# Optimization experiments

Hardware: AMD Instinct MI355X
Metric: run time of the kernel (lower is better)

## Reference

```python
import jax, jax.numpy as jnp
import numpy as np

DIM = 1024
HEADS = 16
DIM_HEAD = 64
SCALE = DIM_HEAD ** -0.5


def setup_inputs() -> dict:
    key = jax.random.key(0)
    ks = jax.random.split(key, 7)
    init = lambda k, shape: jax.random.normal(k, shape, dtype=jnp.float32) * (shape[0] ** -0.5)
    return {
        "x": jax.random.normal(ks[0], (4, 4096, DIM), dtype=jnp.float32),
        "Wq": init(ks[1], (DIM, HEADS * DIM_HEAD)),
        "Wk": init(ks[2], (DIM, HEADS * DIM_HEAD)),
        "Wv": init(ks[3], (DIM, HEADS * DIM_HEAD)),
        "Wg": init(ks[4], (DIM, HEADS * DIM_HEAD)),
        "bg": jnp.zeros((HEADS * DIM_HEAD,), dtype=jnp.float32),
        "Wo": init(ks[5], (HEADS * DIM_HEAD, DIM)),
    }


def _split_heads(t):
    b, n, _ = t.shape
    return t.reshape(b, n, HEADS, DIM_HEAD).transpose(0, 2, 1, 3)  # b h n d


def reference(x, Wq, Wk, Wv, Wg, bg, Wo):
    # projections
    q = _split_heads(x @ Wq)
    k = _split_heads(x @ Wk)
    v = _split_heads(x @ Wv)
    g = _split_heads(x @ Wg + bg)

    # feature map + gate
    q = jax.nn.elu(q) + 1.0
    k = jax.nn.elu(k) + 1.0
    g = jax.nn.sigmoid(g)

    # linear attention: per-head kv state, no n x n scores
    kv = jnp.einsum("bhnd,bhne->bhde", k, v)          # [b,h,d,d]
    k_sum = k.sum(axis=-2)                              # [b,h,d]
    z = 1.0 / jnp.clip(jnp.einsum("bhnd,bhd->bhn", q, k_sum), 1e-6)
    out = jnp.einsum("bhnd,bhde->bhne", q * SCALE, kv)
    out = out * z[..., None] * g                        # [b,h,n,d]

    b, h, n, d = out.shape
    out = out.transpose(0, 2, 1, 3).reshape(b, n, h * d)
    return out @ Wo
```

## Files before the change

### kernel.cpp

```cpp
#include <hip/hip_runtime.h>
#include <math.h>

#define DIM 1024
#define SCALE 0.125f
#define NT 16

typedef __attribute__((ext_vector_type(8))) short bh8;
typedef __attribute__((ext_vector_type(4))) short bh4;
typedef __attribute__((ext_vector_type(4))) float f4v;

__device__ __forceinline__ unsigned short f2bf(float f) {
  unsigned u = __builtin_bit_cast(unsigned, f);
  return (unsigned short)((u + 0x7FFFu + ((u >> 16) & 1u)) >> 16);
}
__device__ __forceinline__ float bf2f(unsigned short u) {
  return __builtin_bit_cast(float, (unsigned)u << 16);
}
__device__ __forceinline__ float elu1(float v) {
  return v > 0.f ? v + 1.f : __expf(v);
}
__device__ __forceinline__ f4v mfma16(bh8 a, bh8 b, f4v c) {
  return __builtin_amdgcn_mfma_f32_16x16x32_bf16(a, b, c, 0, 0, 0);
}

typedef const void __attribute__((address_space(1)))* gas1_t;
typedef void __attribute__((address_space(3)))* las3_t;

__device__ __forceinline__ bh8 frag(const unsigned short* lds, int row, int k8) {
  const int q = ((row << 3) | k8) ^ (row & 7);
  return *reinterpret_cast<const bh8*>(lds + q * 8);
}

__device__ __forceinline__ void gll_tile(const unsigned short* g, int ldg,
                                         unsigned short* lds, int t) {
  const int lane = t & 63, w = t >> 6;
#pragma unroll
  for (int cc = 0; cc < 4; ++cc) {
    const int base = (w * 4 + cc) * 64;
    const int q = base + lane;
    const int c = q ^ ((q >> 3) & 7);
    __builtin_amdgcn_global_load_lds(
        (gas1_t)(const void*)(g + (size_t)(c >> 3) * ldg + (c & 7) * 8),
        (las3_t)(void*)(lds + (size_t)base * 8), 16, 0, 0);
  }
}

__global__ __launch_bounds__(256) void p0(const float* __restrict__ x,
                                          unsigned short* __restrict__ xb) {
  const size_t i = ((size_t)blockIdx.x * 256 + threadIdx.x) * 8;
  const float4 a = *reinterpret_cast<const float4*>(x + i);
  const float4 b = *reinterpret_cast<const float4*>(x + i + 4);
  bh8 v;
  v[0] = (short)f2bf(a.x); v[1] = (short)f2bf(a.y);
  v[2] = (short)f2bf(a.z); v[3] = (short)f2bf(a.w);
  v[4] = (short)f2bf(b.x); v[5] = (short)f2bf(b.y);
  v[6] = (short)f2bf(b.z); v[7] = (short)f2bf(b.w);
  *reinterpret_cast<bh8*>(xb + i) = v;
}

__global__ __launch_bounds__(256) void p1(
    const float* __restrict__ Wq, const float* __restrict__ Wk,
    const float* __restrict__ Wv, const float* __restrict__ Wg,
    const float* __restrict__ Wo, unsigned short* __restrict__ WallT,
    unsigned short* __restrict__ WoT) {
  const int m = blockIdx.z;
  const int tc = blockIdx.x, tr = blockIdx.y;
  const int t = threadIdx.x;
  const float* src = m == 0 ? Wq : m == 1 ? Wk : m == 2 ? Wv : m == 3 ? Wg : Wo;
  __shared__ float tile[64][65];
#pragma unroll
  for (int i = 0; i < 4; ++i) {
    const int idx = i * 256 + t;
    const int r = idx >> 4;
    const int c4 = (idx & 15) * 4;
    const float4 v = *reinterpret_cast<const float4*>(
        src + (size_t)(tr * 64 + r) * DIM + tc * 64 + c4);
    tile[r][c4] = v.x; tile[r][c4 + 1] = v.y;
    tile[r][c4 + 2] = v.z; tile[r][c4 + 3] = v.w;
  }
  __syncthreads();
  unsigned short* dst = (m < 4) ? WallT : WoT;
#pragma unroll
  for (int i = 0; i < 4; ++i) {
    const int idx = i * 256 + t;
    const int lc = idx >> 4;
    const int k4i = (idx & 15) * 4;
    const size_t drow = (m < 4) ? (size_t)(tc * 256 + m * 64 + lc)
                                : (size_t)(tc * 64 + lc);
    bh4 v;
#pragma unroll
    for (int jj = 0; jj < 4; ++jj) v[jj] = (short)f2bf(tile[k4i + jj][lc]);
    *reinterpret_cast<bh4*>(dst + drow * DIM + tr * 64 + k4i) = v;
  }
}

template <int MODE>
__global__ __launch_bounds__(512, 2) void gemm8(
    const unsigned short* __restrict__ gA,
    const unsigned short* __restrict__ gB, const float* __restrict__ bg,
    unsigned short* __restrict__ ob, float* __restrict__ of,
    float* __restrict__ kv_part, float* __restrict__ ksum_part) {
  const int t = threadIdx.x, lane = t & 63, w = t >> 6;
  const int wr = w >> 2, wc = w & 3, g4 = lane >> 4, c0 = lane & 15;
  const int nwg = gridDim.x;
  const int NBC = (MODE == 0) ? 16 : 4;
  const int rbn = nwg / NBC;
  const int bid = (int)blockIdx.x;
  const int xcd = bid & 7;
  const int idx = bid >> 3;
  const int bandsz = rbn >> 3;
  const int cb = idx / bandsz;
  const int rb = xcd * bandsz + (idx - cb * bandsz);

  constexpr int LDGA = (MODE == 0) ? 1024 : 4096;
  constexpr int ASTR = (MODE == 0) ? 64 : 256;
  constexpr int AOFF = (MODE == 0) ? 0 : 64;

  __shared__ __align__(16) unsigned short lds[65536];

  int offA[2], offB[2], dstc[2];
#pragma unroll
  for (int cc = 0; cc < 2; ++cc) {
    const int base = (w * 2 + cc) * 64;
    const int q = base + lane;
    const int c = q ^ ((q >> 3) & 7);
    offA[cc] = (c >> 3) * LDGA + (c & 7) * 8;
    offB[cc] = (c >> 3) * 1024 + (c & 7) * 8;
    dstc[cc] = base * 8;
  }
  const unsigned short* Abase = gA + (size_t)rb * 256 * LDGA + AOFF;
  const unsigned short* Bbase = gB + (size_t)cb * 256 * 1024;

#define SA(kt, half)                                                          \
  {                                                                           \
    _Pragma("unroll") for (int cc = 0; cc < 2; ++cc)                          \
        __builtin_amdgcn_global_load_lds(                                     \
            (gas1_t)(Abase + (size_t)(half) * 128 * LDGA + offA[cc] +         \
                     (kt) * ASTR),                                            \
            (las3_t)(lds + ((kt) & 1) * 16384 + (half) * 8192 + dstc[cc]),    \
            16, 0, 0);                                                        \
  }
#define SB(kt, half)                                                          \
  {                                                                           \
    _Pragma("unroll") for (int cc = 0; cc < 2; ++cc)                          \
        __builtin_amdgcn_global_load_lds(                                     \
            (gas1_t)(Bbase + (size_t)(half) * 128 * 1024 + offB[cc] +         \
                     (kt) * 64),                                              \
            (las3_t)(lds + 32768 + ((kt) & 1) * 16384 + (half) * 8192 +       \
                     dstc[cc]),                                               \
            16, 0, 0);                                                        \
  }

  f4v acc[8][4];
#pragma unroll
  for (int i = 0; i < 8; ++i)
#pragma unroll
    for (int j = 0; j < 4; ++j) acc[i][j] = (f4v){0.f, 0.f, 0.f, 0.f};

  SB(0, 0); SB(0, 1); SA(0, 0); SA(0, 1); SB(1, 0); SB(1, 1);

#pragma unroll 2
  for (int kt = 0; kt < NT; ++kt) {
    if (kt < NT - 1) {
      asm volatile("s_waitcnt vmcnt(4)" ::: "memory");
    } else {
      asm volatile("s_waitcnt vmcnt(0)" ::: "memory");
    }
    __builtin_amdgcn_sched_barrier(0);
    __builtin_amdgcn_s_barrier();
    const unsigned short* Ah = lds + (kt & 1) * 16384 + wr * 8192;
    const unsigned short* Bh =
        lds + 32768 + (kt & 1) * 16384 + (wc >> 1) * 8192;
    const int br0 = (wc & 1) * 64;

    bh8 bfr[4][2], a0[2][2];
#pragma unroll
    for (int nf = 0; nf < 4; ++nf)
#pragma unroll
      for (int kf = 0; kf < 2; ++kf)
        bfr[nf][kf] = frag(Bh, br0 + nf * 16 + c0, kf * 4 + g4);
#pragma unroll
    for (int i = 0; i < 2; ++i)
#pragma unroll
      for (int kf = 0; kf < 2; ++kf)
        a0[i][kf] = frag(Ah, i * 16 + c0, kf * 4 + g4);
    if (kt + 1 < NT) { SA(kt + 1, 0); SA(kt + 1, 1); }
    __builtin_amdgcn_s_barrier();
    __builtin_amdgcn_s_setprio(1);
#pragma unroll
    for (int i = 0; i < 2; ++i)
#pragma unroll
      for (int nf = 0; nf < 4; ++nf)
#pragma unroll
        for (int kf = 0; kf < 2; ++kf)
          acc[i][nf] = mfma16(bfr[nf][kf], a0[i][kf], acc[i][nf]);
    __builtin_amdgcn_s_setprio(0);
    __builtin_amdgcn_s_barrier();

    bh8 a1[2][2];
#pragma unroll
    for (int i = 0; i < 2; ++i)
#pragma unroll
      for (int kf = 0; kf < 2; ++kf)
        a1[i][kf] = frag(Ah, (2 + i) * 16 + c0, kf * 4 + g4);
    if (kt + 2 < NT) SB(kt + 2, 0);
    __builtin_amdgcn_s_barrier();
    __builtin_amdgcn_s_setprio(1);
#pragma unroll
    for (int i = 0; i < 2; ++i)
#pragma unroll
      for (int nf = 0; nf < 4; ++nf)
#pragma unroll
        for (int kf = 0; kf < 2; ++kf)
          acc[2 + i][nf] = mfma16(bfr[nf][kf], a1[i][kf], acc[2 + i][nf]);
    __builtin_amdgcn_s_setprio(0);
    __builtin_amdgcn_s_barrier();

    bh8 a2[2][2];
#pragma unroll
    for (int i = 0; i < 2; ++i)
#pragma unroll
      for (int kf = 0; kf < 2; ++kf)
        a2[i][kf] = frag(Ah, (4 + i) * 16 + c0, kf * 4 + g4);
    if (kt + 2 < NT) SB(kt + 2, 1);
    __builtin_amdgcn_s_barrier();
    __builtin_amdgcn_s_setprio(1);
#pragma unroll
    for (int i = 0; i < 2; ++i)
#pragma unroll
      for (int nf = 0; nf < 4; ++nf)
#pragma unroll
        for (int kf = 0; kf < 2; ++kf)
          acc[4 + i][nf] = mfma16(bfr[nf][kf], a2[i][kf], acc[4 + i][nf]);
    __builtin_amdgcn_s_setprio(0);
    __builtin_amdgcn_s_barrier();

    bh8 a3[2][2];
#pragma unroll
    for (int i = 0; i < 2; ++i)
#pragma unroll
      for (int kf = 0; kf < 2; ++kf)
        a3[i][kf] = frag(Ah, (6 + i) * 16 + c0, kf * 4 + g4);
    __builtin_amdgcn_s_barrier();
    __builtin_amdgcn_s_setprio(1);
#pragma unroll
    for (int i = 0; i < 2; ++i)
#pragma unroll
      for (int nf = 0; nf < 4; ++nf)
#pragma unroll
        for (int kf = 0; kf < 2; ++kf)
          acc[6 + i][nf] = mfma16(bfr[nf][kf], a3[i][kf], acc[6 + i][nf]);
    __builtin_amdgcn_s_setprio(0);
  }
#undef SA
#undef SB

  if (MODE == 0) {
    float bgv[4][4];
    if (wc == 3) {
#pragma unroll
      for (int nf = 0; nf < 4; ++nf) {
        const float4 bv =
            *reinterpret_cast<const float4*>(bg + cb * 64 + nf * 16 + g4 * 4);
        bgv[nf][0] = bv.x; bgv[nf][1] = bv.y;
        bgv[nf][2] = bv.z; bgv[nf][3] = bv.w;
      }
    }
    if (wc == 0 || wc == 3) {
#pragma unroll
      for (int rf = 0; rf < 8; ++rf) {
        const size_t row = (size_t)rb * 256 + wr * 128 + rf * 16 + c0;
#pragma unroll
        for (int nf = 0; nf < 4; ++nf) {
          ushort4 o;
#pragma unroll
          for (int r = 0; r < 4; ++r) {
            float v = acc[rf][nf][r];
            if (wc == 0) v = elu1(v);
            else v = 1.f / (1.f + __expf(-(v + bgv[nf][r])));
            ((unsigned short*)&o)[r] = f2bf(v);
          }
          *reinterpret_cast<ushort4*>(
              ob + row * 4096 + cb * 256 + wc * 64 + nf * 16 + g4 * 4) = o;
        }
      }
    }

    __syncthreads();
    if (wc == 1 || wc == 2) {
      unsigned short* dstT = lds + (wc == 2 ? 16896 : 0);
#pragma unroll
      for (int rf = 0; rf < 8; ++rf) {
        const int n = wr * 128 + rf * 16 + c0;
#pragma unroll
        for (int nf = 0; nf < 4; ++nf)
#pragma unroll
          for (int r = 0; r < 4; ++r) {
            float v = acc[rf][nf][r];
            if (wc == 1) v = elu1(v);
            dstT[(nf * 16 + g4 * 4 + r) * 264 + n] = f2bf(v);
          }
      }
    }
    __syncthreads();
    const unsigned short* kT = lds;
    const unsigned short* vT = lds + 16896;
    const size_t pbase = (size_t)((rb >> 4) * 16 + cb) * 16 + (rb & 15);
#pragma unroll
    for (int pi = 0; pi < 2; ++pi) {
      const int p = w * 2 + pi, dt = p >> 2, et = p & 3;
      f4v a = (f4v){0.f, 0.f, 0.f, 0.f};
#pragma unroll
      for (int kn = 0; kn < 8; ++kn) {
        const bh8 kq = *reinterpret_cast<const bh8*>(
            kT + (dt * 16 + c0) * 264 + kn * 32 + g4 * 8);
        const bh8 vq = *reinterpret_cast<const bh8*>(
            vT + (et * 16 + c0) * 264 + kn * 32 + g4 * 8);
        a = mfma16(vq, kq, a);
      }
      float4 o;
      o.x = a[0]; o.y = a[1]; o.z = a[2]; o.w = a[3];
      *reinterpret_cast<float4*>(
          kv_part + pbase * 4096 + (dt * 16 + c0) * 64 + et * 16 + g4 * 4) = o;
    }
    if (w < 4) {
      bh8 ones;
#pragma unroll
      for (int j = 0; j < 8; ++j) ones[j] = (short)0x3F80;
      f4v a = (f4v){0.f, 0.f, 0.f, 0.f};
#pragma unroll
      for (int kn = 0; kn < 8; ++kn) {
        const bh8 kq = *reinterpret_cast<const bh8*>(
            kT + (w * 16 + c0) * 264 + kn * 32 + g4 * 8);
        a = mfma16(ones, kq, a);
      }
      if (lane < 16) ksum_part[pbase * 64 + w * 16 + c0] = a[0];
    }
  } else {
#pragma unroll
    for (int rf = 0; rf < 8; ++rf) {
      const size_t row = (size_t)rb * 256 + wr * 128 + rf * 16 + c0;
#pragma unroll
      for (int nf = 0; nf < 4; ++nf) {
        float4 o;
        o.x = acc[rf][nf][0]; o.y = acc[rf][nf][1];
        o.z = acc[rf][nf][2]; o.w = acc[rf][nf][3];
        *reinterpret_cast<float4*>(
            of + row * DIM + cb * 256 + wc * 64 + nf * 16 + g4 * 4) = o;
      }
    }
  }
}

__global__ __launch_bounds__(256) void g2r(const float* __restrict__ kv_part,
                                           const float* __restrict__ ksum_part,
                                           unsigned short* __restrict__ kvT,
                                           float* __restrict__ ksum, int b0) {
  const int bhl = blockIdx.x, t = threadIdx.x;
  const size_t bh = (size_t)b0 * 16 + bhl;
#pragma unroll
  for (int i = 0; i < 16; ++i) {
    const int idx = i * 256 + t;
    const int d = idx >> 6, e = idx & 63;
    float s = 0.f;
    for (int sp = 0; sp < 16; ++sp)
      s += kv_part[((size_t)bhl * 16 + sp) * 4096 + idx];
    kvT[bh * 4096 + e * 64 + d] = f2bf(s);
  }
  if (t < 64) {
    float s = 0.f;
    for (int sp = 0; sp < 16; ++sp)
      s += ksum_part[((size_t)bhl * 16 + sp) * 64 + t];
    ksum[bh * 64 + t] = s;
  }
}

__global__ __launch_bounds__(256) void g3(unsigned short* __restrict__ qkvg,
                                          const unsigned short* __restrict__ kvT,
                                          const float* __restrict__ ksum,
                                          int b0) {
  const int h = blockIdx.x, z = blockIdx.y;
  const int t = threadIdx.x, lane = t & 63, w = t >> 6;
  const int g4 = lane >> 4, c0 = lane & 15;
  __shared__ unsigned short sQ[8192];
  __shared__ unsigned short skv[64 * 72];
  __shared__ float sks[64], sden[128];
  const int bb = z >> 5;
  const size_t bh = (size_t)(b0 + bb) * 16 + h;
  for (int i = t; i < 4096; i += 256)
    skv[(i >> 6) * 72 + (i & 63)] = kvT[bh * 4096 + i];
  if (t < 64) sks[t] = ksum[bh * 64 + t];
  const size_t row0 = (size_t)z * 128;
  gll_tile(qkvg + row0 * 4096 + h * 256, 4096, sQ, t);
  __syncthreads();
  {
    const int rr = t >> 1, hf = t & 1;
    float s = 0.f;
#pragma unroll
    for (int dd = 0; dd < 32; ++dd) {
      const int d = hf * 32 + dd;
      s += bf2f(sQ[(((rr << 3) | (d >> 3)) ^ (rr & 7)) * 8 + (d & 7)]) * sks[d];
    }
    s += __shfl_xor(s, 1, 64);
    if (hf == 0) sden[rr] = SCALE / fmaxf(s, 1e-6f);
  }
  __syncthreads();
  f4v oacc[2][4];
#pragma unroll
  for (int ii = 0; ii < 2; ++ii)
#pragma unroll
    for (int et = 0; et < 4; ++et) oacc[ii][et] = (f4v){0.f, 0.f, 0.f, 0.f};
#pragma unroll
  for (int kf = 0; kf < 2; ++kf) {
    bh8 aq[2];
#pragma unroll
    for (int ii = 0; ii < 2; ++ii)
      aq[ii] = frag(sQ, w * 32 + ii * 16 + c0, kf * 4 + g4);
#pragma unroll
    for (int et = 0; et < 4; ++et) {
      const bh8 bkv = *reinterpret_cast<const bh8*>(
          skv + (et * 16 + c0) * 72 + kf * 32 + g4 * 8);
#pragma unroll
      for (int ii = 0; ii < 2; ++ii)
        oacc[ii][et] = mfma16(bkv, aq[ii], oacc[ii][et]);
    }
  }
#pragma unroll
  for (int ii = 0; ii < 2; ++ii) {
    const int n = w * 32 + ii * 16 + c0;
    const float z2 = sden[n];
    const size_t rowbase = (row0 + n) * 4096 + h * 256;
#pragma unroll
    for (int et = 0; et < 4; ++et) {
      const ushort4 gt = *reinterpret_cast<const ushort4*>(
          qkvg + rowbase + 192 + et * 16 + g4 * 4);
      ushort4 o;
#pragma unroll
      for (int r = 0; r < 4; ++r)
        ((unsigned short*)&o)[r] =
            f2bf(oacc[ii][et][r] * z2 * bf2f(((const unsigned short*)&gt)[r]));
      *reinterpret_cast<ushort4*>(qkvg + rowbase + 64 + et * 16 + g4 * 4) = o;
    }
  }
}

extern "C" void kernel_launch(void* const* d_in, const int* in_sizes, int n_in,
                              void* d_out, int out_size, void* d_ws,
                              size_t ws_size, hipStream_t stream) {
  const float* x  = (const float*)d_in[0];
  const float* Wq = (const float*)d_in[1];
  const float* Wk = (const float*)d_in[2];
  const float* Wv = (const float*)d_in[3];
  const float* Wg = (const float*)d_in[4];
  const float* bg = (const float*)d_in[5];
  const float* Wo = (const float*)d_in[6];
  float* out = (float*)d_out;
  char* w = (char*)d_ws;

  const size_t PB = 46202880ull;
  int nbat = 1;
  if (ws_size >= 11026432ull + 4ull * PB) nbat = 4;
  else if (ws_size >= 11026432ull + 2ull * PB) nbat = 2;

  unsigned short* WallT = (unsigned short*)(w);
  unsigned short* WoT   = (unsigned short*)(w + 8388608);
  unsigned short* kvT   = (unsigned short*)(w + 10485760);
  float*          ksum  = (float*)(w + 11010048);
  char* dyn = w + 11026432;
  float* kv_part        = (float*)dyn;
  float* ksum_part      = (float*)(dyn + (size_t)nbat * 4194304);
  unsigned short* xb    = (unsigned short*)(dyn + (size_t)nbat * (4194304 + 65536));
  unsigned short* qkvg  = (unsigned short*)(dyn + (size_t)nbat * (4194304 + 65536 + 8388608));

  p1<<<dim3(16, 16, 5), 256, 0, stream>>>(Wq, Wk, Wv, Wg, Wo, WallT, WoT);

  for (int b0 = 0; b0 < 4; b0 += nbat) {
    const int rows_p = nbat * 4096;
    p0<<<rows_p / 2, 256, 0, stream>>>(x + (size_t)b0 * 4096 * DIM, xb);
    gemm8<0><<<dim3((rows_p / 256) * 16), 512, 0, stream>>>(
        xb, WallT, bg, qkvg, nullptr, kv_part, ksum_part);
    g2r<<<nbat * 16, 256, 0, stream>>>(kv_part, ksum_part, kvT, ksum, b0);
    g3<<<dim3(16, nbat * 32), 256, 0, stream>>>(qkvg, kvT, ksum, b0);
    gemm8<1><<<dim3((rows_p / 256) * 4), 512, 0, stream>>>(
        qkvg, WoT, nullptr, nullptr, out + (size_t)b0 * 4096 * DIM,
        nullptr, nullptr);
  }
}
```

Baseline: 291.3 us.

## Fuse prep kernels, defer q/g stores, halve g3 grid, relax gemm occupancy

Merges the x-to-bf16 conversion and the weight transpose into one launch, with weights handled only on the first batch pass. The q/g epilogue in the projection GEMM now computes values into registers before the kv reduction and stores them afterwards, so the global writes overlap the LDS MFMA work. The g3 kernel now processes two 128-row tiles per block, reusing the kv/ksum loads and halving the grid. gemm8 launch bounds change from 2 to 1 blocks per CU, which allows more registers for the extra qg array but lowers occupancy.

```diff
diff --git a/kernel.cpp b/kernel.cpp
--- a/kernel.cpp
+++ b/kernel.cpp
@@ -45,27 +45,30 @@
   }
 }
 
-__global__ __launch_bounds__(256) void p0(const float* __restrict__ x,
-                                          unsigned short* __restrict__ xb) {
-  const size_t i = ((size_t)blockIdx.x * 256 + threadIdx.x) * 8;
-  const float4 a = *reinterpret_cast<const float4*>(x + i);
-  const float4 b = *reinterpret_cast<const float4*>(x + i + 4);
-  bh8 v;
-  v[0] = (short)f2bf(a.x); v[1] = (short)f2bf(a.y);
-  v[2] = (short)f2bf(a.z); v[3] = (short)f2bf(a.w);
-  v[4] = (short)f2bf(b.x); v[5] = (short)f2bf(b.y);
-  v[6] = (short)f2bf(b.z); v[7] = (short)f2bf(b.w);
-  *reinterpret_cast<bh8*>(xb + i) = v;
-}
-
-__global__ __launch_bounds__(256) void p1(
+__global__ __launch_bounds__(256) void p01(
+    const float* __restrict__ x, unsigned short* __restrict__ xb, int np0,
     const float* __restrict__ Wq, const float* __restrict__ Wk,
     const float* __restrict__ Wv, const float* __restrict__ Wg,
     const float* __restrict__ Wo, unsigned short* __restrict__ WallT,
-    unsigned short* __restrict__ WoT) {
-  const int m = blockIdx.z;
-  const int tc = blockIdx.x, tr = blockIdx.y;
-  const int t = threadIdx.x;
+    unsigned short* __restrict__ WoT, int do_w) {
+  const int bid = (int)blockIdx.x;
+  const int t = (int)threadIdx.x;
+  if (bid < np0) {
+    const size_t i = ((size_t)bid * 256 + t) * 8;
+    const float4 a = *reinterpret_cast<const float4*>(x + i);
+    const float4 b = *reinterpret_cast<const float4*>(x + i + 4);
+    bh8 v;
+    v[0] = (short)f2bf(a.x); v[1] = (short)f2bf(a.y);
+    v[2] = (short)f2bf(a.z); v[3] = (short)f2bf(a.w);
+    v[4] = (short)f2bf(b.x); v[5] = (short)f2bf(b.y);
+    v[6] = (short)f2bf(b.z); v[7] = (short)f2bf(b.w);
+    *reinterpret_cast<bh8*>(xb + i) = v;
+    return;
+  }
+  if (!do_w) return;
+  const int rem = bid - np0;
+  const int m = rem >> 8;
+  const int tc = rem & 15, tr = (rem >> 4) & 15;
   const float* src = m == 0 ? Wq : m == 1 ? Wk : m == 2 ? Wv : m == 3 ? Wg : Wo;
   __shared__ float tile[64][65];
 #pragma unroll
@@ -95,7 +98,7 @@
 }
 
 template <int MODE>
-__global__ __launch_bounds__(512, 2) void gemm8(
+__global__ __launch_bounds__(512, 1) void gemm8(
     const unsigned short* __restrict__ gA,
     const unsigned short* __restrict__ gB, const float* __restrict__ bg,
     unsigned short* __restrict__ ob, float* __restrict__ of,
@@ -266,27 +269,8 @@
         bgv[nf][2] = bv.z; bgv[nf][3] = bv.w;
       }
     }
-    if (wc == 0 || wc == 3) {
-#pragma unroll
-      for (int rf = 0; rf < 8; ++rf) {
-        const size_t row = (size_t)rb * 256 + wr * 128 + rf * 16 + c0;
-#pragma unroll
-        for (int nf = 0; nf < 4; ++nf) {
-          ushort4 o;
-#pragma unroll
-          for (int r = 0; r < 4; ++r) {
-            float v = acc[rf][nf][r];
-            if (wc == 0) v = elu1(v);
-            else v = 1.f / (1.f + __expf(-(v + bgv[nf][r])));
-            ((unsigned short*)&o)[r] = f2bf(v);
-          }
-          *reinterpret_cast<ushort4*>(
-              ob + row * 4096 + cb * 256 + wc * 64 + nf * 16 + g4 * 4) = o;
-        }
-      }
-    }
-
     __syncthreads();
+    ushort4 qg[8][4];
     if (wc == 1 || wc == 2) {
       unsigned short* dstT = lds + (wc == 2 ? 16896 : 0);
 #pragma unroll
@@ -301,6 +285,18 @@
             dstT[(nf * 16 + g4 * 4 + r) * 264 + n] = f2bf(v);
           }
       }
+    } else {
+#pragma unroll
+      for (int rf = 0; rf < 8; ++rf)
+#pragma unroll
+        for (int nf = 0; nf < 4; ++nf)
+#pragma unroll
+          for (int r = 0; r < 4; ++r) {
+            float v = acc[rf][nf][r];
+            if (wc == 0) v = elu1(v);
+            else v = 1.f / (1.f + __expf(-(v + bgv[nf][r])));
+            ((unsigned short*)&qg[rf][nf])[r] = f2bf(v);
+          }
     }
     __syncthreads();
     const unsigned short* kT = lds;
@@ -335,6 +331,17 @@
         a = mfma16(ones, kq, a);
       }
       if (lane < 16) ksum_part[pbase * 64 + w * 16 + c0] = a[0];
+    }
+    if (wc == 0 || wc == 3) {
+#pragma unroll
+      for (int rf = 0; rf < 8; ++rf) {
+        const size_t row = (size_t)rb * 256 + wr * 128 + rf * 16 + c0;
+#pragma unroll
+        for (int nf = 0; nf < 4; ++nf)
+          *reinterpret_cast<ushort4*>(
+              ob + row * 4096 + cb * 256 + wc * 64 + nf * 16 + g4 * 4) =
+              qg[rf][nf];
+      }
     }
   } else {
 #pragma unroll
@@ -385,62 +392,66 @@
   __shared__ unsigned short sQ[8192];
   __shared__ unsigned short skv[64 * 72];
   __shared__ float sks[64], sden[128];
-  const int bb = z >> 5;
+  const int bb = z >> 4;
   const size_t bh = (size_t)(b0 + bb) * 16 + h;
   for (int i = t; i < 4096; i += 256)
     skv[(i >> 6) * 72 + (i & 63)] = kvT[bh * 4096 + i];
   if (t < 64) sks[t] = ksum[bh * 64 + t];
-  const size_t row0 = (size_t)z * 128;
-  gll_tile(qkvg + row0 * 4096 + h * 256, 4096, sQ, t);
-  __syncthreads();
-  {
-    const int rr = t >> 1, hf = t & 1;
-    float s = 0.f;
-#pragma unroll
-    for (int dd = 0; dd < 32; ++dd) {
-      const int d = hf * 32 + dd;
-      s += bf2f(sQ[(((rr << 3) | (d >> 3)) ^ (rr & 7)) * 8 + (d & 7)]) * sks[d];
-    }
-    s += __shfl_xor(s, 1, 64);
-    if (hf == 0) sden[rr] = SCALE / fmaxf(s, 1e-6f);
-  }
-  __syncthreads();
-  f4v oacc[2][4];
-#pragma unroll
-  for (int ii = 0; ii < 2; ++ii)
-#pragma unroll
-    for (int et = 0; et < 4; ++et) oacc[ii][et] = (f4v){0.f, 0.f, 0.f, 0.f};
-#pragma unroll
-  for (int kf = 0; kf < 2; ++kf) {
-    bh8 aq[2];
+  for (int h2 = 0; h2 < 2; ++h2) {
+    const size_t row0 = (size_t)z * 256 + h2 * 128;
+    gll_tile(qkvg + row0 * 4096 + h * 256, 4096, sQ, t);
+    __syncthreads();
+    {
+      const int rr = t >> 1, hf = t & 1;
+      float s = 0.f;
+#pragma unroll
+      for (int dd = 0; dd < 32; ++dd) {
+        const int d = hf * 32 + dd;
+        s += bf2f(sQ[(((rr << 3) | (d >> 3)) ^ (rr & 7)) * 8 + (d & 7)]) *
+             sks[d];
+      }
+      s += __shfl_xor(s, 1, 64);
+      if (hf == 0) sden[rr] = SCALE / fmaxf(s, 1e-6f);
+    }
+    __syncthreads();
+    f4v oacc[2][4];
 #pragma unroll
     for (int ii = 0; ii < 2; ++ii)
-      aq[ii] = frag(sQ, w * 32 + ii * 16 + c0, kf * 4 + g4);
-#pragma unroll
-    for (int et = 0; et < 4; ++et) {
-      const bh8 bkv = *reinterpret_cast<const bh8*>(
-          skv + (et * 16 + c0) * 72 + kf * 32 + g4 * 8);
+#pragma unroll
+      for (int et = 0; et < 4; ++et) oacc[ii][et] = (f4v){0.f, 0.f, 0.f, 0.f};
+#pragma unroll
+    for (int kf = 0; kf < 2; ++kf) {
+      bh8 aq[2];
 #pragma unroll
       for (int ii = 0; ii < 2; ++ii)
-        oacc[ii][et] = mfma16(bkv, aq[ii], oacc[ii][et]);
-    }
-  }
-#pragma unroll
-  for (int ii = 0; ii < 2; ++ii) {
-    const int n = w * 32 + ii * 16 + c0;
-    const float z2 = sden[n];
-    const size_t rowbase = (row0 + n) * 4096 + h * 256;
-#pragma unroll
-    for (int et = 0; et < 4; ++et) {
-      const ushort4 gt = *reinterpret_cast<const ushort4*>(
-          qkvg + rowbase + 192 + et * 16 + g4 * 4);
-      ushort4 o;
-#pragma unroll
-      for (int r = 0; r < 4; ++r)
-        ((unsigned short*)&o)[r] =
-            f2bf(oacc[ii][et][r] * z2 * bf2f(((const unsigned short*)&gt)[r]));
-      *reinterpret_cast<ushort4*>(qkvg + rowbase + 64 + et * 16 + g4 * 4) = o;
-    }
+        aq[ii] = frag(sQ, w * 32 + ii * 16 + c0, kf * 4 + g4);
+#pragma unroll
+      for (int et = 0; et < 4; ++et) {
+        const bh8 bkv = *reinterpret_cast<const bh8*>(
+            skv + (et * 16 + c0) * 72 + kf * 32 + g4 * 8);
+#pragma unroll
+        for (int ii = 0; ii < 2; ++ii)
+          oacc[ii][et] = mfma16(bkv, aq[ii], oacc[ii][et]);
+      }
+    }
+#pragma unroll
+    for (int ii = 0; ii < 2; ++ii) {
+      const int n = w * 32 + ii * 16 + c0;
+      const float z2 = sden[n];
+      const size_t rowbase = (row0 + n) * 4096 + h * 256;
+#pragma unroll
+      for (int et = 0; et < 4; ++et) {
+        const ushort4 gt = *reinterpret_cast<const ushort4*>(
+            qkvg + rowbase + 192 + et * 16 + g4 * 4);
+        ushort4 o;
+#pragma unroll
+        for (int r = 0; r < 4; ++r)
+          ((unsigned short*)&o)[r] =
+              f2bf(oacc[ii][et][r] * z2 * bf2f(((const unsigned short*)&gt)[r]));
+        *reinterpret_cast<ushort4*>(qkvg + rowbase + 64 + et * 16 + g4 * 4) = o;
+      }
+    }
+    __syncthreads();
   }
 }
 
@@ -472,15 +483,16 @@
   unsigned short* xb    = (unsigned short*)(dyn + (size_t)nbat * (4194304 + 65536));
   unsigned short* qkvg  = (unsigned short*)(dyn + (size_t)nbat * (4194304 + 65536 + 8388608));
 
-  p1<<<dim3(16, 16, 5), 256, 0, stream>>>(Wq, Wk, Wv, Wg, Wo, WallT, WoT);
-
   for (int b0 = 0; b0 < 4; b0 += nbat) {
     const int rows_p = nbat * 4096;
-    p0<<<rows_p / 2, 256, 0, stream>>>(x + (size_t)b0 * 4096 * DIM, xb);
+    const int np0 = rows_p / 2;
+    p01<<<np0 + 1280, 256, 0, stream>>>(x + (size_t)b0 * 4096 * DIM, xb, np0,
+                                        Wq, Wk, Wv, Wg, Wo, WallT, WoT,
+                                        b0 == 0 ? 1 : 0);
     gemm8<0><<<dim3((rows_p / 256) * 16), 512, 0, stream>>>(
         xb, WallT, bg, qkvg, nullptr, kv_part, ksum_part);
     g2r<<<nbat * 16, 256, 0, stream>>>(kv_part, ksum_part, kvT, ksum, b0);
-    g3<<<dim3(16, nbat * 32), 256, 0, stream>>>(qkvg, kvT, ksum, b0);
+    g3<<<dim3(16, nbat * 16), 256, 0, stream>>>(qkvg, kvT, ksum, b0);
     gemm8<1><<<dim3((rows_p / 256) * 4), 512, 0, stream>>>(
         qkvg, WoT, nullptr, nullptr, out + (size_t)b0 * 4096 * DIM,
         nullptr, nullptr);
```

New measurement: 275.2 us. -5.6%, faster.
